# Performance work log

Measured on AMD Instinct MI355X. Metric: run time of the kernel, lower is better.

Reference implementation:

```python
import jax, jax.numpy as jnp
import numpy as np


def _knn_graph(x, k):
    """Faithful port of DynamicLstmGnn.knn_to_graph + get_u_v, returning the
    dense symmetrized edge-weight matrix [N, N] (the original re-sparsifies
    this same matrix via coalesce; nonzero extraction is data-dependent and
    not jit-able, so the dense matrix is the canonical output)."""
    N = x.shape[0]
    # negative squared euclidean distance: -||xi||^2 + 2 xi.xj - ||xj||^2
    xx = jnp.sum(x * x, axis=1, keepdims=True)          # [N, 1]
    inner = -2.0 * (x @ x.T)                              # [N, N]
    pairwise_distance = -xx - inner - xx.T                # [N, N], <= 0
    vals, idx = jax.lax.top_k(pairwise_distance, k)       # [N, k] largest (= closest)
    rows = jnp.repeat(jnp.arange(N), k)                   # idx_prime.flatten()
    # sparse COO -> to_dense (duplicate indices sum, matching torch.sparse)
    edges = jnp.zeros((N, N), dtype=x.dtype).at[rows, idx.ravel()].add(vals.ravel())
    edges_int = (edges > 0).astype(x.dtype)
    reflected_int = edges_int + edges_int.T
    reflected_edges = edges + edges.T
    denom = jnp.where(reflected_int == 0, jnp.ones((), x.dtype), reflected_int)
    edges = reflected_edges / denom
    diag = jnp.arange(N)
    edges = edges.at[diag, diag].set(0.0)                 # fill_diagonal_(0)
    return edges


def setup_inputs() -> dict:
    key = jax.random.key(0)
    x = jax.random.normal(key, (10000, 64), dtype=jnp.float32)
    return {"x": x, "k": 5}


def reference(x, k):
    return _knn_graph(x, k)
```

## Files before the change

### kernel.cpp

```cpp
#include <hip/hip_runtime.h>
#include <math.h>
#include <limits.h>

#define D 64
#define K 5
#define LK 8
#define GK 12
#define NSPLIT 16
#define NTILES 625
typedef unsigned int u32;
typedef unsigned long long u64;
typedef __bf16 bf16x8 __attribute__((ext_vector_type(8)));
typedef float  f32x4v __attribute__((ext_vector_type(4)));

__device__ __forceinline__ u32 med3u(u32 a, u32 b, u32 c) {
    u32 r;
    asm("v_med3_u32 %0, %1, %2, %3" : "=v"(r) : "v"(a), "v"(b), "v"(c));
    return r;
}

__device__ __forceinline__ u32 pack32(float v, int idx) {
    u32 u = __float_as_uint(v);
    u ^= ((u32)((int)u >> 31)) | 0x80000000u;
    return (u & 0xFFFFC000u) | ((~(u32)idx) & 0x3FFFu);
}
__device__ __forceinline__ int idx32(u32 key) { return (int)((~key) & 0x3FFFu); }

__device__ __forceinline__ u64 packKV(float v, int idx) {
    u32 u = __float_as_uint(v);
    u ^= ((u32)((int)u >> 31)) | 0x80000000u;
    return ((u64)u << 32) | (u32)(~idx);
}
__device__ __forceinline__ float unpackV(u64 key) {
    u32 hu = (u32)(key >> 32);
    return (hu & 0x80000000u) ? __uint_as_float(hu & 0x7fffffffu)
                              : __uint_as_float(~hu);
}

template<int LO, int LA, int LB, typename T>
__device__ __forceinline__ void mergeKeep(T a[LA], const T b[LB]) {
    T A[LA], B[LB], out[LO];
#pragma unroll
    for (int i = 0; i < LA; ++i) A[i] = a[i];
#pragma unroll
    for (int i = 0; i < LB; ++i) B[i] = b[i];
#pragma unroll
    for (int m = 0; m < LO; ++m) {
        bool ta = A[0] >= B[0];
        out[m] = ta ? A[0] : B[0];
#pragma unroll
        for (int i = 0; i < LA - 1; ++i) A[i] = ta ? A[i + 1] : A[i];
        A[LA - 1] = ta ? (T)0 : A[LA - 1];
#pragma unroll
        for (int i = 0; i < LB - 1; ++i) B[i] = ta ? B[i] : B[i + 1];
        B[LB - 1] = ta ? B[LB - 1] : (T)0;
    }
#pragma unroll
    for (int m = 0; m < LO; ++m) a[m] = out[m];
}

__global__ __launch_bounds__(256) void prep(
    const float* __restrict__ x, __bf16* __restrict__ xbA, float* __restrict__ xxf, int N)
{
    int g = blockIdx.x * 256 + threadIdx.x;
    const int REPACK = NTILES * 2 * 64;
    if (g < REPACK) {
        int tile = g >> 7;
        int rem  = g & 127;
        int kh   = rem >> 6;
        int lane = rem & 63;
        int q = lane >> 4, r = lane & 15;
        int row = tile * 16 + r;
        int k0  = kh * 32 + q * 8;
        const float4* p = (const float4*)(x + (size_t)row * D + k0);
        float4 v0 = p[0], v1 = p[1];
        bf16x8 o;
        o[0] = (__bf16)v0.x; o[1] = (__bf16)v0.y; o[2] = (__bf16)v0.z; o[3] = (__bf16)v0.w;
        o[4] = (__bf16)v1.x; o[5] = (__bf16)v1.y; o[6] = (__bf16)v1.z; o[7] = (__bf16)v1.w;
        ((bf16x8*)xbA)[g] = o;
        return;
    }
    int i = g - REPACK;
    if (i >= N) return;
    const float4* p = (const float4*)(x + (size_t)i * D);
    float s = 0.f;
#pragma unroll
    for (int t = 0; t < 16; ++t) {
        float4 v = p[t];
        s += v.x * v.x + v.y * v.y + v.z * v.z + v.w * v.w;
    }
    xxf[i] = s;
}

__global__ __launch_bounds__(256) void topk_mfma(
    const __bf16* __restrict__ xbA, const float* __restrict__ xxf, int N,
    u32* __restrict__ wsK, float* __restrict__ outZ, long long totalF4, int f4PerBlock)
{
    const int tid  = threadIdx.x;
    const int lane = tid & 63;
    const int wave = tid >> 6;
    const int l15  = lane & 15;
    const int q    = lane >> 4;
    const int split = blockIdx.y;
    const int r0 = blockIdx.x * 64 + wave * 16;

    const int bid = split * gridDim.x + blockIdx.x;
    long long zcur = (long long)bid * f4PerBlock;
    long long zend = zcur + f4PerBlock; if (zend > totalF4) zend = totalF4;
    const int nIters = (NTILES - split + NSPLIT - 1) / NSPLIT;
    const long long zChunk = (f4PerBlock + nIters - 1) / nIters;

    const bf16x8* fb = (const bf16x8*)xbA;

    int bt = r0 >> 4; if (bt > NTILES - 1) bt = NTILES - 1;
    const bf16x8 B0 = fb[bt * 128 + lane];
    const bf16x8 B1 = fb[bt * 128 + 64 + lane];

    const bf16x8* ap = fb + (size_t)split * 128 + lane;
    const float* xcp = xxf + split * 16 + q * 4;
    int cbase = split * 16 + q * 4;
    const int apBump = NSPLIT * 128;
    const int xcBump = NSPLIT * 16;

    u32 L[LK];
#pragma unroll
    for (int m = 0; m < LK; ++m) L[m] = 0u;

    for (int t = split; t < NTILES; t += NSPLIT) {
        const bf16x8 A0 = ap[0];
        const bf16x8 A1 = ap[64];
        const f32x4v xc = *(const f32x4v*)xcp;
        ap += apBump;
        xcp += xcBump;

        {
            long long e = zcur + zChunk; if (e > zend) e = zend;
            const f32x4v z = {0.f, 0.f, 0.f, 0.f};
            for (long long i = zcur + tid; i < e; i += 256)
                __builtin_nontemporal_store(z, (f32x4v*)(outZ + 4 * i));
            zcur += zChunk;
        }

        f32x4v acc = {0.f, 0.f, 0.f, 0.f};
        acc = __builtin_amdgcn_mfma_f32_16x16x32_bf16(A0, B0, acc, 0, 0, 0);
        acc = __builtin_amdgcn_mfma_f32_16x16x32_bf16(A1, B1, acc, 0, 0, 0);

#pragma unroll
        for (int v = 0; v < 4; ++v) {
            float dk = fmaf(-0.5f, xc[v], acc[v]);
            u32 key = pack32(dk, cbase + v);
            u32 n0 = max(L[0], key);
            u32 n1 = med3u(L[0], L[1], key);
            u32 n2 = med3u(L[1], L[2], key);
            u32 n3 = med3u(L[2], L[3], key);
            u32 n4 = med3u(L[3], L[4], key);
            u32 n5 = med3u(L[4], L[5], key);
            u32 n6 = med3u(L[5], L[6], key);
            u32 n7 = med3u(L[6], L[7], key);
            L[0]=n0; L[1]=n1; L[2]=n2; L[3]=n3; L[4]=n4; L[5]=n5; L[6]=n6; L[7]=n7;
        }
        cbase += xcBump;
    }

#pragma unroll
    for (int mask = 16; mask <= 32; mask <<= 1) {
        u32 P[LK];
#pragma unroll
        for (int m = 0; m < LK; ++m) P[m] = (u32)__shfl_xor((int)L[m], mask);
        mergeKeep<LK, LK, LK, u32>(L, P);
    }

    if (lane < 16) {
        int row = r0 + l15;
        if (row < N) {
            u32* dst = wsK + ((size_t)row * NSPLIT + split) * LK;
#pragma unroll
            for (int m = 0; m < LK; ++m) dst[m] = L[m];
        }
    }
}

__global__ __launch_bounds__(256) void rescore_scatter(
    const u32* __restrict__ wsK, const float* __restrict__ x, const float* __restrict__ xxf,
    float* __restrict__ out, int N)
{
    const int lane = threadIdx.x & 63;
    const int wave = threadIdx.x >> 6;
    const int sub  = lane & 3;
    const int row  = blockIdx.x * 64 + wave * 16 + (lane >> 2);
    const bool vrow = (row < N);
    const int rr = vrow ? row : 0;

    u32 cur[GK];
    {
        const u32* Lp = wsK + ((size_t)rr * NSPLIT + 4 * sub) * LK;
#pragma unroll
        for (int m = 0; m < LK; ++m) cur[m] = Lp[m];
#pragma unroll
        for (int m = LK; m < GK; ++m) cur[m] = 0u;
#pragma unroll
        for (int l = 1; l < 4; ++l) {
            u32 b[LK];
#pragma unroll
            for (int m = 0; m < LK; ++m) b[m] = Lp[l * LK + m];
            mergeKeep<GK, GK, LK, u32>(cur, b);
        }
    }
#pragma unroll
    for (int mask = 1; mask <= 2; mask <<= 1) {
        u32 P[GK];
#pragma unroll
        for (int m = 0; m < GK; ++m) P[m] = (u32)__shfl_xor((int)cur[m], mask);
        mergeKeep<GK, GK, GK, u32>(cur, P);
    }

    const float nxi = xxf[rr];
    int   cj[3]; bool cval[3];
    float d[3] = {0.f, 0.f, 0.f};
    const f32x4v* pj[3];
#pragma unroll
    for (int c = 0; c < 3; ++c) {
        int j = idx32(cur[sub * 3 + c]);
        cval[c] = (j < N) && (cur[sub * 3 + c] != 0u);
        cj[c] = cval[c] ? j : 0;
        pj[c] = (const f32x4v*)(x + (size_t)cj[c] * D);
    }
    const f32x4v* xip = (const f32x4v*)(x + (size_t)rr * D);
#pragma unroll
    for (int t = 0; t < 16; ++t) {
        const f32x4v xv = xip[t];
#pragma unroll
        for (int c = 0; c < 3; ++c) {
            const f32x4v pv = pj[c][t];
            d[c] = fmaf(xv[0], pv[0], d[c]);
            d[c] = fmaf(xv[1], pv[1], d[c]);
            d[c] = fmaf(xv[2], pv[2], d[c]);
            d[c] = fmaf(xv[3], pv[3], d[c]);
        }
    }
    u64 F[K];
#pragma unroll
    for (int c = 0; c < 3; ++c) {
        float val = 2.f * d[c] - nxi - xxf[cj[c]];
        F[c] = cval[c] ? packKV(val, cj[c]) : 0ull;
    }
    F[3] = 0ull; F[4] = 0ull;
    { u64 a0=F[0],a1=F[1],a2=F[2];
      if (a0 < a1) { u64 t0=a0; a0=a1; a1=t0; }
      if (a1 < a2) { u64 t0=a1; a1=a2; a2=t0; }
      if (a0 < a1) { u64 t0=a0; a0=a1; a1=t0; }
      F[0]=a0; F[1]=a1; F[2]=a2; }
#pragma unroll
    for (int mask = 1; mask <= 2; mask <<= 1) {
        u64 P[K];
#pragma unroll
        for (int m = 0; m < K; ++m) P[m] = __shfl_xor(F[m], mask);
        mergeKeep<K, K, K, u64>(F, P);
    }

    if (sub == 0 && vrow) {
#pragma unroll
        for (int m = 0; m < K; ++m) {
            int j = (int)(~(u32)F[m]);
            if ((unsigned)j < (unsigned)N && j != row) {
                float v = unpackV(F[m]);
                atomicAdd(out + (size_t)row * N + j, v);
                atomicAdd(out + (size_t)j * N + row, v);
            }
        }
    }
}

extern "C" void kernel_launch(void* const* d_in, const int* in_sizes, int n_in,
                              void* d_out, int out_size, void* d_ws, size_t ws_size,
                              hipStream_t stream) {
    const float* x = (const float*)d_in[0];
    const int N = in_sizes[0] / D;
    float* out = (float*)d_out;

    const size_t oXB = 0;
    const size_t oXX = ((size_t)NTILES * 2 * 64 * 8 * 2 + 255) & ~255ull;
    const size_t oWK = (oXX + (size_t)N * 4 + 255) & ~255ull;
    __bf16* xbA = (__bf16*)((char*)d_ws + oXB);
    float*  xxf = (float*)((char*)d_ws + oXX);
    u32*    wsK = (u32*)((char*)d_ws + oWK);

    const int prepThreads = NTILES * 2 * 64 + N;
    prep<<<(prepThreads + 255) / 256, 256, 0, stream>>>(x, xbA, xxf, N);

    const int rowBlocks = (N + 63) / 64;
    dim3 grid(rowBlocks, NSPLIT);
    long long totalF4 = (long long)out_size / 4;
    int nBlocks = rowBlocks * NSPLIT;
    int f4PerBlock = (int)((totalF4 + nBlocks - 1) / nBlocks);
    topk_mfma<<<grid, 256, 0, stream>>>(xbA, xxf, N, wsK, out, totalF4, f4PerBlock);

    rescore_scatter<<<rowBlocks, 256, 0, stream>>>(wsK, x, xxf, out, N);
}
```

Baseline: 475.7 us.

## Split output zeroing into dedicated blocks interleaved with top-k compute blocks

Before, every top-k block zeroed a slice of the dense output inside its main tile loop. Now a flat grid sends every sixth block to pure non-temporal zero stores, and the other blocks run only the MFMA distance and top-k work. The aim is to take the store loop out of the compute loop and let the two kinds of work overlap across CUs. The trade-off is that each zeroing block must now stream a large contiguous chunk by itself, which could leave write bandwidth unevenly spread. The grid size and row-block count are also hardcoded for N=10000.

```diff
diff --git a/kernel.cpp b/kernel.cpp
--- a/kernel.cpp
+++ b/kernel.cpp
@@ -8,6 +8,8 @@
 #define GK 12
 #define NSPLIT 16
 #define NTILES 625
+#define ROWBLK 157
+#define NCOMP (ROWBLK * NSPLIT)
 typedef unsigned int u32;
 typedef unsigned long long u64;
 typedef __bf16 bf16x8 __attribute__((ext_vector_type(8)));
@@ -92,23 +94,35 @@
     xxf[i] = s;
 }
 
-__global__ __launch_bounds__(256) void topk_mfma(
+__global__ __launch_bounds__(256) void topk_zero_mfma(
     const __bf16* __restrict__ xbA, const float* __restrict__ xxf, int N,
-    u32* __restrict__ wsK, float* __restrict__ outZ, long long totalF4, int f4PerBlock)
+    u32* __restrict__ wsK, float* __restrict__ outZ, long long totalF4,
+    int nZero, int f4PerZ)
 {
-    const int tid  = threadIdx.x;
+    const int bx  = blockIdx.x;
+    const int tid = threadIdx.x;
+
+    if (bx % 6 == 0) {
+        int zid = bx / 6;
+        if (zid >= nZero) return;
+        long long s = (long long)zid * f4PerZ;
+        long long e = s + f4PerZ; if (e > totalF4) e = totalF4;
+        const f32x4v z = {0.f, 0.f, 0.f, 0.f};
+        for (long long i = s + tid; i < e; i += 256)
+            __builtin_nontemporal_store(z, (f32x4v*)(outZ + 4 * i));
+        return;
+    }
+
+    const int cid = bx - (bx / 6 + 1);
+    if (cid >= NCOMP) return;
+    const int split = cid / ROWBLK;
+    const int rb    = cid - split * ROWBLK;
+
     const int lane = tid & 63;
     const int wave = tid >> 6;
     const int l15  = lane & 15;
     const int q    = lane >> 4;
-    const int split = blockIdx.y;
-    const int r0 = blockIdx.x * 64 + wave * 16;
-
-    const int bid = split * gridDim.x + blockIdx.x;
-    long long zcur = (long long)bid * f4PerBlock;
-    long long zend = zcur + f4PerBlock; if (zend > totalF4) zend = totalF4;
-    const int nIters = (NTILES - split + NSPLIT - 1) / NSPLIT;
-    const long long zChunk = (f4PerBlock + nIters - 1) / nIters;
+    const int r0 = rb * 64 + wave * 16;
 
     const bf16x8* fb = (const bf16x8*)xbA;
 
@@ -132,14 +146,6 @@
         const f32x4v xc = *(const f32x4v*)xcp;
         ap += apBump;
         xcp += xcBump;
-
-        {
-            long long e = zcur + zChunk; if (e > zend) e = zend;
-            const f32x4v z = {0.f, 0.f, 0.f, 0.f};
-            for (long long i = zcur + tid; i < e; i += 256)
-                __builtin_nontemporal_store(z, (f32x4v*)(outZ + 4 * i));
-            zcur += zChunk;
-        }
 
         f32x4v acc = {0.f, 0.f, 0.f, 0.f};
         acc = __builtin_amdgcn_mfma_f32_16x16x32_bf16(A0, B0, acc, 0, 0, 0);
@@ -288,12 +294,12 @@
     const int prepThreads = NTILES * 2 * 64 + N;
     prep<<<(prepThreads + 255) / 256, 256, 0, stream>>>(x, xbA, xxf, N);
 
-    const int rowBlocks = (N + 63) / 64;
-    dim3 grid(rowBlocks, NSPLIT);
     long long totalF4 = (long long)out_size / 4;
-    int nBlocks = rowBlocks * NSPLIT;
-    int f4PerBlock = (int)((totalF4 + nBlocks - 1) / nBlocks);
-    topk_mfma<<<grid, 256, 0, stream>>>(xbA, xxf, N, wsK, out, totalF4, f4PerBlock);
-
-    rescore_scatter<<<rowBlocks, 256, 0, stream>>>(wsK, x, xxf, out, N);
-}
+    const int nBlocksTotal = 3024;
+    const int nZero = (nBlocksTotal + 5) / 6;
+    int f4PerZ = (int)((totalF4 + nZero - 1) / nZero);
+    topk_zero_mfma<<<nBlocksTotal, 256, 0, stream>>>(
+        xbA, xxf, N, wsK, out, totalF4, nZero, f4PerZ);
+
+    rescore_scatter<<<ROWBLK, 256, 0, stream>>>(wsK, x, xxf, out, N);
+}
```

Result: faster. 451.2 us (median of 2 runs) (-5.1%).
